# Kernel tuning notes

Hardware: AMD Instinct MI355X
Metric: run time of the kernel (lower is better)

Reference implementation:

```python
import jax, jax.numpy as jnp
import numpy as np

BZ, C, H, W = 8, 512, 64, 64


def setup_inputs() -> dict:
    key = jax.random.key(0)
    x = jax.random.normal(key, (BZ, C, H, W), dtype=jnp.float32)
    # central square hole: flag==1 -> masked (unknown), flag==0 -> known
    mask = np.zeros((H, W), dtype=np.int32)
    mask[H // 4: 3 * H // 4, W // 4: 3 * W // 4] = 1
    return {"x": x, "mask": jnp.asarray(mask)}


def reference(x, mask):
    # InnerShiftSingle forward with shift_sz=1, stride=1, mask_thred=1:
    # flag == feature-level mask (each 1x1 patch is masked iff its pixel is masked).
    bz, c, h, w = x.shape
    c2 = c // 2
    hw = h * w
    flag = mask.reshape(hw)  # [hw] int, 1=masked, 0=known

    former = x[:, :c2]   # decoder features [b,c2,h,w]
    latter = x[:, c2:]   # encoder features [b,c2,h,w]

    former_f = former.reshape(bz, c2, hw).transpose(0, 2, 1)  # [b,hw,c2]
    latter_f = latter.reshape(bz, c2, hw).transpose(0, 2, 1)  # [b,hw,c2]

    # original: conv of (un-normalized) former with L2-normalized latter 1x1 patches
    latter_n = latter_f / (jnp.linalg.norm(latter_f, axis=-1, keepdims=True) + 1e-8)
    cosine = jnp.einsum('bpc,bqc->bpq', former_f, latter_n)  # [b,hw,hw]
    # only known-region patches (flag==0) are candidate sources
    cosine = jnp.where(flag[None, None, :] == 1, -jnp.inf, cosine)

    best = jnp.argmax(cosine, axis=-1)  # [b,hw] index into known region
    shift = jnp.take_along_axis(latter_f, best[..., None], axis=1)  # [b,hw,c2]
    # only masked positions receive a shifted feature; known positions stay 0
    shift = jnp.where(flag[None, :, None] == 1, shift, jnp.zeros((), x.dtype))
    shift = shift.transpose(0, 2, 1).reshape(bz, c2, h, w)

    return jnp.concatenate([former, latter, shift], axis=1)  # [b, 3c/2, h, w]
```

## Files before the change

### kernel.cpp

```cpp
#include <hip/hip_runtime.h>
#include <math.h>

#define BZc 8
#define Cc 512
#define C2c 256
#define HWc 4096
#define OUTC 768
#define NP 1024
#define NQ 3072
#define QG 8
#define TAU 5e-5f
#define FIXSLOTS 64

typedef _Float16 h8 __attribute__((ext_vector_type(8)));
typedef float f16v __attribute__((ext_vector_type(16)));
typedef float f32x4 __attribute__((ext_vector_type(4)));

__device__ __forceinline__ void glds16(const void* g, void* l) {
    __builtin_amdgcn_global_load_lds(
        (const __attribute__((address_space(1))) void*)g,
        (__attribute__((address_space(3))) void*)l, 16, 0, 0);
}

__global__ __launch_bounds__(1024) void k_build(const int* __restrict__ mask,
                                                int* __restrict__ pidx,
                                                int* __restrict__ qinv,
                                                int* __restrict__ pinv,
                                                int* __restrict__ cnt) {
    __shared__ int s0[1024], s1[1024], t0[1024], t1[1024];
    int t = threadIdx.x;
    if (t < 8) cnt[t] = 0;
    int f[4];
    int cp = 0;
#pragma unroll
    for (int j = 0; j < 4; ++j) { f[j] = mask[t * 4 + j]; cp += f[j]; }
    s0[t] = cp; s1[t] = 4 - cp;
    __syncthreads();
    int *a = s0, *b = s1, *c = t0, *d = t1;
    for (int off = 1; off < 1024; off <<= 1) {
        int vp = a[t] + (t >= off ? a[t - off] : 0);
        int vq = b[t] + (t >= off ? b[t - off] : 0);
        c[t] = vp; d[t] = vq;
        __syncthreads();
        int* tmp;
        tmp = a; a = c; c = tmp;
        tmp = b; b = d; d = tmp;
    }
    int ep = a[t] - cp;
    int eq = b[t] - (4 - cp);
#pragma unroll
    for (int j = 0; j < 4; ++j) {
        int idx = t * 4 + j;
        if (f[j]) { pidx[ep] = idx; pinv[idx] = ep; qinv[idx] = -1; ep++; }
        else      { qinv[idx] = eq; pinv[idx] = -1; eq++; }
    }
}

__global__ __launch_bounds__(256) void k_prep(const float* __restrict__ x,
                                              const int* __restrict__ pinv,
                                              const int* __restrict__ qinv,
                                              _Float16* __restrict__ latH,
                                              _Float16* __restrict__ latL,
                                              _Float16* __restrict__ forH,
                                              _Float16* __restrict__ forL,
                                              float* __restrict__ invn,
                                              float* __restrict__ invnC,
                                              float* __restrict__ out) {
    int id = blockIdx.x;
    bool isLat = id < 1024;
    int rid = isLat ? id : id - 1024;
    int b = rid >> 7;
    int g = rid & 127;
    int col0 = g * 32;
    int tid = threadIdx.x;
    __shared__ float tile[64][33];
    __shared__ float ssq[32][33];
    __shared__ int rowm[32];
    if (tid < 32) rowm[tid] = isLat ? qinv[col0 + tid] : pinv[col0 + tid];
    const float* xb = x + (size_t)b * Cc * HWc + (isLat ? (size_t)C2c * HWc : 0);
    float* ob = out + (size_t)b * OUTC * HWc + (isLat ? (size_t)C2c * HWc : 0);
    _Float16* dH = isLat ? latH + (size_t)b * NQ * 256 : forH + (size_t)b * NP * 256;
    _Float16* dL = isLat ? latL + (size_t)b * NQ * 256 : forL + (size_t)b * NP * 256;

    int cr = tid >> 3;
    int c4 = (tid & 7) * 4;

    f32x4 vv[4][2];
#pragma unroll
    for (int c = 0; c < 4; ++c) {
        vv[c][0] = *(const f32x4*)(xb + (size_t)(c * 64 + cr) * HWc + col0 + c4);
        vv[c][1] = *(const f32x4*)(xb + (size_t)(c * 64 + 32 + cr) * HWc + col0 + c4);
    }
    __syncthreads();

    int qq = tid >> 3, sub = tid & 7;
    int dr = rowm[qq];

#pragma unroll
    for (int c = 0; c < 4; ++c) {
        {
            f32x4 v0 = vv[c][0], v1 = vv[c][1];
            tile[cr][c4]      = v0.x; tile[cr][c4 + 1]      = v0.y;
            tile[cr][c4 + 2]  = v0.z; tile[cr][c4 + 3]      = v0.w;
            tile[32 + cr][c4] = v1.x; tile[32 + cr][c4 + 1] = v1.y;
            tile[32 + cr][c4 + 2] = v1.z; tile[32 + cr][c4 + 3] = v1.w;
        }
        __syncthreads();
        if (dr >= 0) {
            h8 hv, lv;
#pragma unroll
            for (int j = 0; j < 8; ++j) {
                float v = tile[sub * 8 + j][qq];
                _Float16 h = (_Float16)v;
                hv[j] = h; lv[j] = (_Float16)((v - (float)h) * 2048.0f);
            }
            int slot = c * 8 + sub;
            int dslot = isLat ? (slot ^ (dr & 31)) : slot;
            size_t o = (size_t)dr * 256 + dslot * 8;
            *(h8*)(dH + o) = hv;
            *(h8*)(dL + o) = lv;
        }
        __syncthreads();
    }

#pragma unroll
    for (int c = 0; c < 4; ++c) {
        *(f32x4*)(ob + (size_t)(c * 64 + cr) * HWc + col0 + c4) = vv[c][0];
        *(f32x4*)(ob + (size_t)(c * 64 + 32 + cr) * HWc + col0 + c4) = vv[c][1];
    }

    if (isLat) {
        float s0 = 0.f, s1 = 0.f, s2 = 0.f, s3 = 0.f;
#pragma unroll
        for (int c = 0; c < 4; ++c)
#pragma unroll
            for (int p = 0; p < 2; ++p) {
                f32x4 v = vv[c][p];
                s0 = fmaf(v.x, v.x, s0); s1 = fmaf(v.y, v.y, s1);
                s2 = fmaf(v.z, v.z, s2); s3 = fmaf(v.w, v.w, s3);
            }
        ssq[cr][c4] = s0; ssq[cr][c4 + 1] = s1; ssq[cr][c4 + 2] = s2; ssq[cr][c4 + 3] = s3;
        __syncthreads();
        if (tid < 32) {
            float s = 0.f;
#pragma unroll
            for (int r = 0; r < 32; ++r) s += ssq[r][tid];
            float inv = 1.0f / (sqrtf(s) + 1e-8f);
            invn[b * HWc + col0 + tid] = inv;
            int qc = rowm[tid];
            if (qc >= 0) invnC[b * NQ + qc] = inv;
        }
    } else {
        f32x4 z = {0.f, 0.f, 0.f, 0.f};
        float* sb = out + (size_t)b * OUTC * HWc + (size_t)Cc * HWc;
        for (int i = tid; i < 256 * 8; i += 256) {
            int ch = i >> 3, j4 = i & 7;
            *(f32x4*)(sb + (size_t)ch * HWc + col0 + j4 * 4) = z;
        }
    }
}

__global__ __launch_bounds__(512, 2) void k_gemm(const _Float16* __restrict__ latH,
                                                 const _Float16* __restrict__ latL,
                                                 const _Float16* __restrict__ forH,
                                                 const _Float16* __restrict__ forL,
                                                 const float* __restrict__ invnC,
                                                 float* __restrict__ bv1,
                                                 int* __restrict__ bi1,
                                                 float* __restrict__ bv2) {
    int pg = blockIdx.x;
    int qg = blockIdx.y;
    int b  = blockIdx.z;
    int tid = threadIdx.x;
    int w = tid >> 6, lane = tid & 63;
    int l31 = lane & 31, lh = lane >> 5;

    __shared__ __align__(16) _Float16 sH[2][32 * 256];
    __shared__ __align__(16) _Float16 sL[2][32 * 256];
    __shared__ float sInv[384];

    if (tid < 384) sInv[tid] = invnC[b * NQ + qg * 384 + tid];

    size_t fo = ((size_t)(b * NP + pg * 256 + w * 32 + l31)) * 256 + lh * 8;
    const _Float16* fH = forH + fo;
    const _Float16* fL = forL + fo;
    h8 BH[16], BL[16];
#pragma unroll
    for (int ks = 0; ks < 16; ++ks) {
        BH[ks] = *(const h8*)(fH + ks * 16);
        BL[ks] = *(const h8*)(fL + ks * 16);
    }

    const _Float16* latHb = latH + (size_t)(b * NQ + qg * 384) * 256;
    const _Float16* latLb = latL + (size_t)(b * NQ + qg * 384) * 256;

#define STAGE(bf, tt)                                                              \
    {                                                                              \
        const char* gH = (const char*)(latHb + (size_t)(tt) * 32 * 256);           \
        const char* gL = (const char*)(latLb + (size_t)(tt) * 32 * 256);           \
        char* lH = (char*)&sH[bf][0];                                              \
        char* lL = (char*)&sL[bf][0];                                              \
        int go = w * 2048 + lane * 16;                                             \
        int lo = w * 2048;                                                         \
        glds16(gH + go, lH + lo);                                                  \
        glds16(gH + go + 1024, lH + lo + 1024);                                    \
        glds16(gL + go, lL + lo);                                                  \
        glds16(gL + go + 1024, lL + lo + 1024);                                    \
    }

    const int offc[16] = {0,1,2,3,8,9,10,11,16,17,18,19,24,25,26,27};
    float v1 = -INFINITY, v2 = -INFINITY; int i1 = 0;

    STAGE(0, 0);
    __syncthreads();

    for (int t = 0; t < 12; ++t) {
        if (t < 11) STAGE((t + 1) & 1, t + 1);
        const _Float16* bufH = &sH[t & 1][0];
        const _Float16* bufL = &sL[t & 1][0];
        f16v accA = {}, accB = {};
#pragma unroll
        for (int ks = 0; ks < 16; ++ks) {
            int slotA = (ks * 2 + lh) ^ l31;
            h8 aH = *(const h8*)(bufH + l31 * 256 + slotA * 8);
            h8 aL = *(const h8*)(bufL + l31 * 256 + slotA * 8);
            accA = __builtin_amdgcn_mfma_f32_32x32x16_f16(aH, BH[ks], accA, 0, 0, 0);
            accB = __builtin_amdgcn_mfma_f32_32x32x16_f16(aH, BL[ks], accB, 0, 0, 0);
            accB = __builtin_amdgcn_mfma_f32_32x32x16_f16(aL, BH[ks], accB, 0, 0, 0);
        }
        int qb = qg * 384 + t * 32 + 4 * lh;
        float val[16];
#pragma unroll
        for (int r = 0; r < 16; ++r)
            val[r] = (accA[r] + accB[r] * (1.0f / 2048.0f)) * sInv[t * 32 + 4 * lh + offc[r]];
        float n1[8], n2[8]; int ni[8];
#pragma unroll
        for (int s = 0; s < 8; ++s) {
            float va = val[2 * s], vb = val[2 * s + 1];
            bool bw = vb > va;
            n1[s] = bw ? vb : va;
            ni[s] = qb + (bw ? offc[2 * s + 1] : offc[2 * s]);
            n2[s] = bw ? va : vb;
        }
#pragma unroll
        for (int lvl = 4; lvl >= 1; lvl >>= 1) {
#pragma unroll
            for (int s = 0; s < 8; ++s) {
                if (s < lvl) {
                    float av = n1[2 * s], bv = n1[2 * s + 1];
                    bool bw = bv > av;
                    float m1 = bw ? bv : av;
                    int   mi = bw ? ni[2 * s + 1] : ni[2 * s];
                    float m2 = fmaxf(fmaxf(n2[2 * s], n2[2 * s + 1]), bw ? av : bv);
                    n1[s] = m1; ni[s] = mi; n2[s] = m2;
                }
            }
        }
        {
            bool bw = n1[0] > v1;
            v2 = fmaxf(fmaxf(v2, n2[0]), bw ? v1 : n1[0]);
            if (bw) { v1 = n1[0]; i1 = ni[0]; }
        }
        __syncthreads();
    }
#undef STAGE
    float ov1 = __shfl_xor(v1, 32);
    int   oi1 = __shfl_xor(i1, 32);
    float ov2 = __shfl_xor(v2, 32);
    if (ov1 > v1) { v2 = fmaxf(v1, ov2); v1 = ov1; i1 = oi1; }
    else          { v2 = fmaxf(ov1, v2); }
    if (lane < 32) {
        size_t o = ((size_t)b * NP + pg * 256 + w * 32 + lane) * QG + qg;
        bv1[o] = v1; bi1[o] = i1; bv2[o] = v2;
    }
}

__global__ void k_reduce(const float* __restrict__ bv1, const int* __restrict__ bi1,
                         const float* __restrict__ bv2, int* __restrict__ bfin,
                         int* __restrict__ cnt, int* __restrict__ fixrows) {
    int t = blockIdx.x * blockDim.x + threadIdx.x;
    if (t >= BZc * NP) return;
    float V1 = -INFINITY, V2 = -INFINITY; int I1 = 0;
    for (int c = 0; c < QG; ++c) {
        float a = bv1[(size_t)t * QG + c];
        float a2 = bv2[(size_t)t * QG + c];
        int   i = bi1[(size_t)t * QG + c];
        if (a > V1) { V2 = fmaxf(V1, a2); V1 = a; I1 = i; }
        else        { V2 = fmaxf(V2, a); }
    }
    bfin[t] = I1;
    if (V1 - V2 < TAU) {
        int b = t >> 10;
        int s = atomicAdd(&cnt[b], 1);
        if (s < FIXSLOTS) fixrows[b * FIXSLOTS + s] = t & 1023;
    }
}

__global__ __launch_bounds__(256) void k_fixA(const float* __restrict__ x,
                                              const int* __restrict__ pidx,
                                              const int* __restrict__ mask,
                                              const float* __restrict__ invn,
                                              const int* __restrict__ cnt,
                                              const int* __restrict__ fixrows,
                                              float* __restrict__ fixv,
                                              int* __restrict__ fixi) {
    int qg = blockIdx.x, s = blockIdx.y, b = blockIdx.z;
    int n = cnt[b]; if (n > FIXSLOTS) n = FIXSLOTS;
    if (s >= n) return;
    int p = fixrows[b * FIXSLOTS + s];
    int porig = pidx[p];
    int tid = threadIdx.x;
    __shared__ float fs[256];
    fs[tid] = x[((size_t)b * Cc + tid) * HWc + porig];
    __syncthreads();
    const float* lx = x + ((size_t)b * Cc + C2c) * HWc;
    int q0 = qg * 1024 + tid * 4;
    float4 acc = make_float4(0.f, 0.f, 0.f, 0.f);
    for (int c0 = 0; c0 < 256; c0 += 8) {
        float4 v[8];
#pragma unroll
        for (int u = 0; u < 8; ++u)
            v[u] = *(const float4*)(lx + (size_t)(c0 + u) * HWc + q0);
#pragma unroll
        for (int u = 0; u < 8; ++u) {
            float fc = fs[c0 + u];
            acc.x = fmaf(fc, v[u].x, acc.x);
            acc.y = fmaf(fc, v[u].y, acc.y);
            acc.z = fmaf(fc, v[u].z, acc.z);
            acc.w = fmaf(fc, v[u].w, acc.w);
        }
    }
    float vals[4] = {acc.x, acc.y, acc.z, acc.w};
    float bv = -INFINITY; int bq = 1 << 30;
#pragma unroll
    for (int k = 0; k < 4; ++k) {
        int q = q0 + k;
        float val = vals[k] * invn[b * HWc + q];
        if (mask[q] == 0 && val > bv) { bv = val; bq = q; }
    }
    __shared__ float rv[256]; __shared__ int rq[256];
    rv[tid] = bv; rq[tid] = bq; __syncthreads();
    for (int off = 128; off > 0; off >>= 1) {
        if (tid < off) {
            float v2 = rv[tid + off]; int q2 = rq[tid + off];
            if (v2 > rv[tid] || (v2 == rv[tid] && q2 < rq[tid])) { rv[tid] = v2; rq[tid] = q2; }
        }
        __syncthreads();
    }
    if (tid == 0) {
        fixv[(b * FIXSLOTS + s) * 4 + qg] = rv[0];
        fixi[(b * FIXSLOTS + s) * 4 + qg] = rq[0];
    }
}

__global__ void k_fixB(const int* __restrict__ cnt, const int* __restrict__ fixrows,
                       const float* __restrict__ fixv, const int* __restrict__ fixi,
                       const int* __restrict__ qinv, int* __restrict__ bfin) {
    int t = threadIdx.x;
    int b = t >> 6, s = t & 63;
    int n = cnt[b]; if (n > FIXSLOTS) n = FIXSLOTS;
    if (s >= n) return;
    float bv = -INFINITY; int bq = 1 << 30;
    for (int qg = 0; qg < 4; ++qg) {
        float v = fixv[(b * FIXSLOTS + s) * 4 + qg];
        int   q = fixi[(b * FIXSLOTS + s) * 4 + qg];
        if (v > bv || (v == bv && q < bq)) { bv = v; bq = q; }
    }
    int p = fixrows[b * FIXSLOTS + s];
    bfin[b * NP + p] = qinv[bq];
}

__global__ __launch_bounds__(256) void k_scatter(const _Float16* __restrict__ latH,
                                                 const _Float16* __restrict__ latL,
                                                 const int* __restrict__ bfin,
                                                 const int* __restrict__ pidx,
                                                 float* __restrict__ out) {
    int blk = blockIdx.x;
    int b   = blockIdx.y;
    int tid = threadIdx.x;
    __shared__ float tile[32][257];
    __shared__ int qd[32], pd[32];
    if (tid < 32) {
        qd[tid] = bfin[b * NP + blk * 32 + tid];
        pd[tid] = pidx[blk * 32 + tid];
    }
    __syncthreads();
    for (int i = tid; i < 32 * 256; i += 256) {
        int pp = i >> 8, c = i & 255;
        int q = qd[pp];
        int slot = c >> 3;
        size_t o = ((size_t)b * NQ + q) * 256 + ((slot ^ (q & 31)) << 3) + (c & 7);
        tile[pp][c] = (float)latH[o] + (float)latL[o] * (1.0f / 2048.0f);
    }
    __syncthreads();
    float* ob = out + (size_t)b * OUTC * HWc + (size_t)Cc * HWc;
    for (int i = tid; i < 256 * 32; i += 256) {
        int ch = i >> 5, j = i & 31;
        ob[(size_t)ch * HWc + pd[j]] = tile[j][ch];
    }
}

extern "C" void kernel_launch(void* const* d_in, const int* in_sizes, int n_in,
                              void* d_out, int out_size, void* d_ws, size_t ws_size,
                              hipStream_t stream) {
    const float* x    = (const float*)d_in[0];
    const int*   mask = (const int*)d_in[1];
    float* out = (float*)d_out;
    char*  ws  = (char*)d_ws;

    _Float16* latH = (_Float16*)(ws);
    _Float16* latL = (_Float16*)(ws + 12582912);
    _Float16* forH = (_Float16*)(ws + 25165824);
    _Float16* forL = (_Float16*)(ws + 29360128);
    float* invn    = (float*)(ws + 33554432);
    float* invnC   = (float*)(ws + 33685504);
    float* bv1     = (float*)(ws + 33783808);
    int*   bi1     = (int*)  (ws + 34045952);
    float* bv2     = (float*)(ws + 34308096);
    int*   bfin    = (int*)  (ws + 34570240);
    int*   pidx    = (int*)  (ws + 34603008);
    int*   qinv    = (int*)  (ws + 34607104);
    int*   pinv    = (int*)  (ws + 34623488);
    int*   cnt     = (int*)  (ws + 34639872);
    int*   fixrows = (int*)  (ws + 34639904);
    float* fixv    = (float*)(ws + 34641952);
    int*   fixi    = (int*)  (ws + 34650144);

    k_build<<<1, 1024, 0, stream>>>(mask, pidx, qinv, pinv, cnt);
    k_prep<<<2048, 256, 0, stream>>>(x, pinv, qinv, latH, latL, forH, forL, invn, invnC, out);
    k_gemm<<<dim3(4, QG, BZc), 512, 0, stream>>>(latH, latL, forH, forL, invnC, bv1, bi1, bv2);
    k_reduce<<<(BZc * NP + 255) / 256, 256, 0, stream>>>(bv1, bi1, bv2, bfin, cnt, fixrows);
    k_fixA<<<dim3(4, FIXSLOTS, BZc), 256, 0, stream>>>(x, pidx, mask, invn, cnt, fixrows, fixv, fixi);
    k_fixB<<<1, 512, 0, stream>>>(cnt, fixrows, fixv, fixi, qinv, bfin);
    k_scatter<<<dim3(32, BZc), 256, 0, stream>>>(latH, latL, bfin, pidx, out);
}
```

Before: 115.1 us.

## Split GEMM query range across twice as many blocks with half-K LDS staging

```diff
diff --git a/kernel.cpp b/kernel.cpp
--- a/kernel.cpp
+++ b/kernel.cpp
@@ -8,7 +8,7 @@
 #define OUTC 768
 #define NP 1024
 #define NQ 3072
-#define QG 8
+#define QG 16
 #define TAU 5e-5f
 #define FIXSLOTS 64
 
@@ -115,7 +115,7 @@
                 hv[j] = h; lv[j] = (_Float16)((v - (float)h) * 2048.0f);
             }
             int slot = c * 8 + sub;
-            int dslot = isLat ? (slot ^ (dr & 31)) : slot;
+            int dslot = isLat ? (slot ^ (dr & 15)) : slot;
             size_t o = (size_t)dr * 256 + dslot * 8;
             *(h8*)(dH + o) = hv;
             *(h8*)(dL + o) = lv;
@@ -175,11 +175,11 @@
     int w = tid >> 6, lane = tid & 63;
     int l31 = lane & 31, lh = lane >> 5;
 
-    __shared__ __align__(16) _Float16 sH[2][32 * 256];
-    __shared__ __align__(16) _Float16 sL[2][32 * 256];
-    __shared__ float sInv[384];
-
-    if (tid < 384) sInv[tid] = invnC[b * NQ + qg * 384 + tid];
+    __shared__ __align__(16) _Float16 sH[2][32 * 128];
+    __shared__ __align__(16) _Float16 sL[2][32 * 128];
+    __shared__ float sInv[192];
+
+    if (tid < 192) sInv[tid] = invnC[b * NQ + qg * 192 + tid];
 
     size_t fo = ((size_t)(b * NP + pg * 256 + w * 32 + l31)) * 256 + lh * 8;
     const _Float16* fH = forH + fo;
@@ -191,48 +191,51 @@
         BL[ks] = *(const h8*)(fL + ks * 16);
     }
 
-    const _Float16* latHb = latH + (size_t)(b * NQ + qg * 384) * 256;
-    const _Float16* latLb = latL + (size_t)(b * NQ + qg * 384) * 256;
-
-#define STAGE(bf, tt)                                                              \
+    const _Float16* latHb = latH + (size_t)(b * NQ + qg * 192) * 256;
+    const _Float16* latLb = latL + (size_t)(b * NQ + qg * 192) * 256;
+
+#define STAGE(bf, qt, kh)                                                          \
     {                                                                              \
-        const char* gH = (const char*)(latHb + (size_t)(tt) * 32 * 256);           \
-        const char* gL = (const char*)(latLb + (size_t)(tt) * 32 * 256);           \
-        char* lH = (char*)&sH[bf][0];                                              \
-        char* lL = (char*)&sL[bf][0];                                              \
-        int go = w * 2048 + lane * 16;                                             \
-        int lo = w * 2048;                                                         \
-        glds16(gH + go, lH + lo);                                                  \
-        glds16(gH + go + 1024, lH + lo + 1024);                                    \
-        glds16(gL + go, lL + lo);                                                  \
-        glds16(gL + go + 1024, lL + lo + 1024);                                    \
+        const char* gH = (const char*)latHb + (size_t)(qt) * 16384 + (kh) * 256;   \
+        const char* gL = (const char*)latLb + (size_t)(qt) * 16384 + (kh) * 256;   \
+        char* lH = (char*)&sH[bf][0] + w * 1024;                                   \
+        char* lL = (char*)&sL[bf][0] + w * 1024;                                   \
+        int go = (w * 4 + (lane >> 4)) * 512 + (lane & 15) * 16;                   \
+        glds16(gH + go, lH);                                                       \
+        glds16(gL + go, lL);                                                       \
     }
 
     const int offc[16] = {0,1,2,3,8,9,10,11,16,17,18,19,24,25,26,27};
     float v1 = -INFINITY, v2 = -INFINITY; int i1 = 0;
 
-    STAGE(0, 0);
-    __syncthreads();
-
-    for (int t = 0; t < 12; ++t) {
-        if (t < 11) STAGE((t + 1) & 1, t + 1);
-        const _Float16* bufH = &sH[t & 1][0];
-        const _Float16* bufL = &sL[t & 1][0];
+    STAGE(0, 0, 0);
+    __syncthreads();
+
+    for (int qt = 0; qt < 6; ++qt) {
         f16v accA = {}, accB = {};
 #pragma unroll
-        for (int ks = 0; ks < 16; ++ks) {
-            int slotA = (ks * 2 + lh) ^ l31;
-            h8 aH = *(const h8*)(bufH + l31 * 256 + slotA * 8);
-            h8 aL = *(const h8*)(bufL + l31 * 256 + slotA * 8);
-            accA = __builtin_amdgcn_mfma_f32_32x32x16_f16(aH, BH[ks], accA, 0, 0, 0);
-            accB = __builtin_amdgcn_mfma_f32_32x32x16_f16(aH, BL[ks], accB, 0, 0, 0);
-            accB = __builtin_amdgcn_mfma_f32_32x32x16_f16(aL, BH[ks], accB, 0, 0, 0);
-        }
-        int qb = qg * 384 + t * 32 + 4 * lh;
+        for (int kh = 0; kh < 2; ++kh) {
+            int t = qt * 2 + kh;
+            if (t < 11) { int tn = t + 1; STAGE(tn & 1, tn >> 1, tn & 1); }
+            const _Float16* bufH = &sH[t & 1][0];
+            const _Float16* bufL = &sL[t & 1][0];
+#pragma unroll
+            for (int ks = 0; ks < 8; ++ks) {
+                int phys = (ks * 2 + lh) ^ (l31 & 15);
+                h8 aH = *(const h8*)(bufH + l31 * 128 + phys * 8);
+                h8 aL = *(const h8*)(bufL + l31 * 128 + phys * 8);
+                int bj = kh * 8 + ks;
+                accA = __builtin_amdgcn_mfma_f32_32x32x16_f16(aH, BH[bj], accA, 0, 0, 0);
+                accB = __builtin_amdgcn_mfma_f32_32x32x16_f16(aH, BL[bj], accB, 0, 0, 0);
+                accB = __builtin_amdgcn_mfma_f32_32x32x16_f16(aL, BH[bj], accB, 0, 0, 0);
+            }
+            if (kh == 0) __syncthreads();
+        }
+        int qb = qg * 192 + qt * 32 + 4 * lh;
         float val[16];
 #pragma unroll
         for (int r = 0; r < 16; ++r)
-            val[r] = (accA[r] + accB[r] * (1.0f / 2048.0f)) * sInv[t * 32 + 4 * lh + offc[r]];
+            val[r] = (accA[r] + accB[r] * (1.0f / 2048.0f)) * sInv[qt * 32 + 4 * lh + offc[r]];
         float n1[8], n2[8]; int ni[8];
 #pragma unroll
         for (int s = 0; s < 8; ++s) {
@@ -388,8 +391,8 @@
     for (int i = tid; i < 32 * 256; i += 256) {
         int pp = i >> 8, c = i & 255;
         int q = qd[pp];
-        int slot = c >> 3;
-        size_t o = ((size_t)b * NQ + q) * 256 + ((slot ^ (q & 31)) << 3) + (c & 7);
+        int dslot = (c >> 3) ^ (q & 15);
+        size_t o = ((size_t)b * NQ + q) * 256 + (dslot << 3) + (c & 7);
         tile[pp][c] = (float)latH[o] + (float)latL[o] * (1.0f / 2048.0f);
     }
     __syncthreads();
@@ -415,16 +418,16 @@
     float* invn    = (float*)(ws + 33554432);
     float* invnC   = (float*)(ws + 33685504);
     float* bv1     = (float*)(ws + 33783808);
-    int*   bi1     = (int*)  (ws + 34045952);
-    float* bv2     = (float*)(ws + 34308096);
-    int*   bfin    = (int*)  (ws + 34570240);
-    int*   pidx    = (int*)  (ws + 34603008);
-    int*   qinv    = (int*)  (ws + 34607104);
-    int*   pinv    = (int*)  (ws + 34623488);
-    int*   cnt     = (int*)  (ws + 34639872);
-    int*   fixrows = (int*)  (ws + 34639904);
-    float* fixv    = (float*)(ws + 34641952);
-    int*   fixi    = (int*)  (ws + 34650144);
+    int*   bi1     = (int*)  (ws + 34308096);
+    float* bv2     = (float*)(ws + 34832384);
+    int*   bfin    = (int*)  (ws + 35356672);
+    int*   pidx    = (int*)  (ws + 35389440);
+    int*   qinv    = (int*)  (ws + 35393536);
+    int*   pinv    = (int*)  (ws + 35409920);
+    int*   cnt     = (int*)  (ws + 35426304);
+    int*   fixrows = (int*)  (ws + 35426336);
+    float* fixv    = (float*)(ws + 35428384);
+    int*   fixi    = (int*)  (ws + 35436576);
 
     k_build<<<1, 1024, 0, stream>>>(mask, pidx, qinv, pinv, cnt);
     k_prep<<<2048, 256, 0, stream>>>(x, pinv, qinv, latH, latL, forH, forL, invn, invnC, out);
```

Result: slower. 124.4 us (+8.1%).

## Store latter features slot-major and read GEMM A operand directly from global

Applied to the files above, without the earlier changes.

```diff
diff --git a/kernel.cpp b/kernel.cpp
--- a/kernel.cpp
+++ b/kernel.cpp
@@ -15,12 +15,6 @@
 typedef _Float16 h8 __attribute__((ext_vector_type(8)));
 typedef float f16v __attribute__((ext_vector_type(16)));
 typedef float f32x4 __attribute__((ext_vector_type(4)));
-
-__device__ __forceinline__ void glds16(const void* g, void* l) {
-    __builtin_amdgcn_global_load_lds(
-        (const __attribute__((address_space(1))) void*)g,
-        (__attribute__((address_space(3))) void*)l, 16, 0, 0);
-}
 
 __global__ __launch_bounds__(1024) void k_build(const int* __restrict__ mask,
                                                 int* __restrict__ pidx,
@@ -115,8 +109,8 @@
                 hv[j] = h; lv[j] = (_Float16)((v - (float)h) * 2048.0f);
             }
             int slot = c * 8 + sub;
-            int dslot = isLat ? (slot ^ (dr & 31)) : slot;
-            size_t o = (size_t)dr * 256 + dslot * 8;
+            size_t o = isLat ? ((size_t)slot * NQ + dr) * 8
+                             : ((size_t)dr * 256 + slot * 8);
             *(h8*)(dH + o) = hv;
             *(h8*)(dL + o) = lv;
         }
@@ -160,7 +154,7 @@
     }
 }
 
-__global__ __launch_bounds__(512, 2) void k_gemm(const _Float16* __restrict__ latH,
+__global__ __launch_bounds__(256, 2) void k_gemm(const _Float16* __restrict__ latH,
                                                  const _Float16* __restrict__ latL,
                                                  const _Float16* __restrict__ forH,
                                                  const _Float16* __restrict__ forL,
@@ -175,13 +169,11 @@
     int w = tid >> 6, lane = tid & 63;
     int l31 = lane & 31, lh = lane >> 5;
 
-    __shared__ __align__(16) _Float16 sH[2][32 * 256];
-    __shared__ __align__(16) _Float16 sL[2][32 * 256];
-    __shared__ float sInv[384];
-
-    if (tid < 384) sInv[tid] = invnC[b * NQ + qg * 384 + tid];
-
-    size_t fo = ((size_t)(b * NP + pg * 256 + w * 32 + l31)) * 256 + lh * 8;
+    __shared__ float sInvA[384];
+    for (int i = tid; i < 384; i += 256) sInvA[i] = invnC[b * NQ + qg * 384 + i];
+    __syncthreads();
+
+    size_t fo = ((size_t)(b * NP + pg * 128 + w * 32 + l31)) * 256 + lh * 8;
     const _Float16* fH = forH + fo;
     const _Float16* fL = forL + fo;
     h8 BH[16], BL[16];
@@ -191,48 +183,38 @@
         BL[ks] = *(const h8*)(fL + ks * 16);
     }
 
-    const _Float16* latHb = latH + (size_t)(b * NQ + qg * 384) * 256;
-    const _Float16* latLb = latL + (size_t)(b * NQ + qg * 384) * 256;
-
-#define STAGE(bf, tt)                                                              \
-    {                                                                              \
-        const char* gH = (const char*)(latHb + (size_t)(tt) * 32 * 256);           \
-        const char* gL = (const char*)(latLb + (size_t)(tt) * 32 * 256);           \
-        char* lH = (char*)&sH[bf][0];                                              \
-        char* lL = (char*)&sL[bf][0];                                              \
-        int go = w * 2048 + lane * 16;                                             \
-        int lo = w * 2048;                                                         \
-        glds16(gH + go, lH + lo);                                                  \
-        glds16(gH + go + 1024, lH + lo + 1024);                                    \
-        glds16(gL + go, lL + lo);                                                  \
-        glds16(gL + go + 1024, lL + lo + 1024);                                    \
-    }
+    const _Float16* AH = latH + (size_t)b * NQ * 256;
+    const _Float16* AL = latL + (size_t)b * NQ * 256;
 
     const int offc[16] = {0,1,2,3,8,9,10,11,16,17,18,19,24,25,26,27};
     float v1 = -INFINITY, v2 = -INFINITY; int i1 = 0;
 
-    STAGE(0, 0);
-    __syncthreads();
-
     for (int t = 0; t < 12; ++t) {
-        if (t < 11) STAGE((t + 1) & 1, t + 1);
-        const _Float16* bufH = &sH[t & 1][0];
-        const _Float16* bufL = &sL[t & 1][0];
-        f16v accA = {}, accB = {};
-#pragma unroll
-        for (int ks = 0; ks < 16; ++ks) {
-            int slotA = (ks * 2 + lh) ^ l31;
-            h8 aH = *(const h8*)(bufH + l31 * 256 + slotA * 8);
-            h8 aL = *(const h8*)(bufL + l31 * 256 + slotA * 8);
-            accA = __builtin_amdgcn_mfma_f32_32x32x16_f16(aH, BH[ks], accA, 0, 0, 0);
-            accB = __builtin_amdgcn_mfma_f32_32x32x16_f16(aH, BL[ks], accB, 0, 0, 0);
-            accB = __builtin_amdgcn_mfma_f32_32x32x16_f16(aL, BH[ks], accB, 0, 0, 0);
+        int qrow = qg * 384 + t * 32 + l31;
+        f16v accA = {}, accB0 = {}, accB1 = {};
+#pragma unroll
+        for (int kb = 0; kb < 4; ++kb) {
+            h8 ah[4], al[4];
+#pragma unroll
+            for (int j = 0; j < 4; ++j) {
+                int s = (kb * 4 + j) * 2 + lh;
+                ah[j] = *(const h8*)(AH + ((size_t)s * NQ + qrow) * 8);
+                al[j] = *(const h8*)(AL + ((size_t)s * NQ + qrow) * 8);
+            }
+#pragma unroll
+            for (int j = 0; j < 4; ++j) {
+                int bj = kb * 4 + j;
+                accA  = __builtin_amdgcn_mfma_f32_32x32x16_f16(ah[j], BH[bj], accA, 0, 0, 0);
+                accB0 = __builtin_amdgcn_mfma_f32_32x32x16_f16(ah[j], BL[bj], accB0, 0, 0, 0);
+                accB1 = __builtin_amdgcn_mfma_f32_32x32x16_f16(al[j], BH[bj], accB1, 0, 0, 0);
+            }
         }
         int qb = qg * 384 + t * 32 + 4 * lh;
         float val[16];
 #pragma unroll
         for (int r = 0; r < 16; ++r)
-            val[r] = (accA[r] + accB[r] * (1.0f / 2048.0f)) * sInv[t * 32 + 4 * lh + offc[r]];
+            val[r] = (accA[r] + (accB0[r] + accB1[r]) * (1.0f / 2048.0f))
+                     * sInvA[t * 32 + 4 * lh + offc[r]];
         float n1[8], n2[8]; int ni[8];
 #pragma unroll
         for (int s = 0; s < 8; ++s) {
@@ -261,16 +243,14 @@
             v2 = fmaxf(fmaxf(v2, n2[0]), bw ? v1 : n1[0]);
             if (bw) { v1 = n1[0]; i1 = ni[0]; }
         }
-        __syncthreads();
-    }
-#undef STAGE
+    }
     float ov1 = __shfl_xor(v1, 32);
     int   oi1 = __shfl_xor(i1, 32);
     float ov2 = __shfl_xor(v2, 32);
     if (ov1 > v1) { v2 = fmaxf(v1, ov2); v1 = ov1; i1 = oi1; }
     else          { v2 = fmaxf(ov1, v2); }
     if (lane < 32) {
-        size_t o = ((size_t)b * NP + pg * 256 + w * 32 + lane) * QG + qg;
+        size_t o = ((size_t)b * NP + pg * 128 + w * 32 + lane) * QG + qg;
         bv1[o] = v1; bi1[o] = i1; bv2[o] = v2;
     }
 }
@@ -385,12 +365,13 @@
         pd[tid] = pidx[blk * 32 + tid];
     }
     __syncthreads();
+    const _Float16* AH = latH + (size_t)b * NQ * 256;
+    const _Float16* AL = latL + (size_t)b * NQ * 256;
     for (int i = tid; i < 32 * 256; i += 256) {
         int pp = i >> 8, c = i & 255;
         int q = qd[pp];
-        int slot = c >> 3;
-        size_t o = ((size_t)b * NQ + q) * 256 + ((slot ^ (q & 31)) << 3) + (c & 7);
-        tile[pp][c] = (float)latH[o] + (float)latL[o] * (1.0f / 2048.0f);
+        size_t o = ((size_t)(c >> 3) * NQ + q) * 8 + (c & 7);
+        tile[pp][c] = (float)AH[o] + (float)AL[o] * (1.0f / 2048.0f);
     }
     __syncthreads();
     float* ob = out + (size_t)b * OUTC * HWc + (size_t)Cc * HWc;
@@ -428,7 +409,7 @@
 
     k_build<<<1, 1024, 0, stream>>>(mask, pidx, qinv, pinv, cnt);
     k_prep<<<2048, 256, 0, stream>>>(x, pinv, qinv, latH, latL, forH, forL, invn, invnC, out);
-    k_gemm<<<dim3(4, QG, BZc), 512, 0, stream>>>(latH, latL, forH, forL, invnC, bv1, bi1, bv2);
+    k_gemm<<<dim3(8, QG, BZc), 256, 0, stream>>>(latH, latL, forH, forL, invnC, bv1, bi1, bv2);
     k_reduce<<<(BZc * NP + 255) / 256, 256, 0, stream>>>(bv1, bi1, bv2, bfin, cnt, fixrows);
     k_fixA<<<dim3(4, FIXSLOTS, BZc), 256, 0, stream>>>(x, pidx, mask, invn, cnt, fixrows, fixv, fixi);
     k_fixB<<<1, 512, 0, stream>>>(cnt, fixrows, fixv, fixi, qinv, bfin);
```

New measurement: 202.2 us. 1.76x slower.
